# Optimization experiments

Measured on AMD Instinct MI355X. Metric: run time of the kernel, lower is better.

Reference implementation:

```python
import jax, jax.numpy as jnp
import numpy as np

B, NPG, IN_DIM, HID, H, DEG, NTYPE, NLAYERS = 4, 5000, 16, 128, 8, 32, 12, 4
N = B * NPG
DH = HID // H
E = N * DEG + N  # random edges + self loops


def setup_inputs() -> dict:
    key = jax.random.key(0)
    ks = jax.random.split(key, 10)
    e_rand = N * DEG
    # intra-graph random edges: sample within [0, NPG) then offset by graph id
    src = jax.random.randint(ks[0], (e_rand,), 0, NPG, dtype=jnp.int32)
    dst = jax.random.randint(ks[1], (e_rand,), 0, NPG, dtype=jnp.int32)
    gid = jnp.repeat(jnp.arange(B, dtype=jnp.int32), NPG * DEG) * NPG
    loops = jnp.arange(N, dtype=jnp.int32)
    edge_index = jnp.stack([jnp.concatenate([src + gid, loops]),
                            jnp.concatenate([dst + gid, loops])])
    edge_type = jnp.concatenate([
        jax.random.randint(ks[2], (e_rand,), 1, NTYPE, dtype=jnp.int32),
        jnp.zeros((N,), jnp.int32)])  # self-loop type = 0
    feat = jax.random.normal(ks[3], (N, IN_DIM), jnp.float32)
    s = 0.1
    return {
        "feat": feat,
        "edge_table": jax.random.normal(ks[4], (NTYPE, HID), jnp.float32) * s,
        "W_embed": jax.random.normal(ks[5], (IN_DIM, HID), jnp.float32) * s,
        "b_embed": jnp.zeros((HID,), jnp.float32),
        "W_conv": jax.random.normal(ks[6], (HID, HID), jnp.float32) * s,
        "a_src": jax.random.normal(ks[7], (H, DH), jnp.float32) * s,
        "a_dst": jax.random.normal(ks[8], (H, DH), jnp.float32) * s,
        "a_edge": jax.random.normal(ks[9], (H, DH), jnp.float32) * s,
        "edge_index": edge_index,
        "edge_type": edge_type,
    }


def _forward(feat, edge_table, W_embed, b_embed, W_conv, a_src, a_dst, a_edge,
             edge_index, edge_type):
    src, dst = edge_index[0], edge_index[1]
    # feature masking done in the torch forward
    feat = feat.at[:, 2:4].set(0.0).at[:, 10:].set(0.0)
    # 'sum'-flavor edge embedding: type lookup -> [E, H, DH]
    e_feat = edge_table[edge_type].reshape(-1, H, DH)
    ea = jnp.sum(e_feat * a_edge, axis=-1)  # [E, H]
    h = jax.nn.gelu(feat @ W_embed + b_embed)  # node embedder MLP
    layers = [feat, h]
    for _ in range(NLAYERS):  # shared_conv=True: same weights each layer
        z = (h @ W_conv).reshape(N, H, DH)
        s_logit = jnp.sum(z * a_src, axis=-1)  # [N, H]
        d_logit = jnp.sum(z * a_dst, axis=-1)
        logit = jax.nn.leaky_relu(s_logit[src] + d_logit[dst] + ea, 0.2)
        # numerically-stable edge softmax over incoming edges of each dst
        m = jax.ops.segment_max(logit, dst, num_segments=N)
        ex = jnp.exp(logit - jax.lax.stop_gradient(m)[dst])
        denom = jax.ops.segment_sum(ex, dst, num_segments=N)
        alpha = ex / (denom[dst] + 1e-9)  # [E, H]
        msg = alpha[..., None] * z[src]  # [E, H, DH]
        agg = jax.ops.segment_sum(msg, dst, num_segments=N).reshape(N, HID)
        h = h + jax.nn.gelu(agg)  # residual
        layers.append(h)
    feats_all = jnp.concatenate(layers, axis=1)  # layer_pooling='all' -> [N, 656]
    nf = feats_all.reshape(B, NPG, -1)
    g_emb = jnp.max(nf, axis=1, keepdims=True)  # graph_pooling='max'
    return jnp.concatenate([nf, jnp.broadcast_to(g_emb, nf.shape)], axis=2)


def reference(feat, edge_table, W_embed, b_embed, W_conv, a_src, a_dst, a_edge,
              edge_index, edge_type):
    return _forward(feat, edge_table, W_embed, b_embed, W_conv, a_src, a_dst,
                    a_edge, edge_index, edge_type)
```

## Files before the change

kernel.cpp:

```cpp
#include <hip/hip_runtime.h>
#include <math.h>

#define IN_DIM 16
#define HIDN 128
#define NH 8
#define DHD 16
#define NTYPE 12
#define NLAYERS 4
#define NPG 5000
#define NSEGP 250
#define RPS (NPG / NSEGP)
#define C1 656
#define C2 1312
#define C1Q (C1 / 4)
#define CAP 64
#define NPW 4
#define HREG (NPG / 2)
#define GEMM_SLOTS ((HREG + 63) / 64)
#define EDGE_SLOTS (HREG / NPW)

__device__ __forceinline__ float gelu_t(float x) {
    float x3 = x * x * x;
    float u = 0.7978845608028654f * (x + 0.044715f * x3);
    return 0.5f * x * (1.0f + tanhf(u));
}

__device__ __forceinline__ unsigned pack_bf16(float lo, float hi) {
    unsigned a = __float_as_uint(lo);
    unsigned b = __float_as_uint(hi);
    a = (a + 0x7fffu + ((a >> 16) & 1u)) >> 16;
    b = (b + 0x7fffu + ((b >> 16) & 1u)) & 0xffff0000u;
    return a | b;
}

__device__ __forceinline__ float lrelu(float x) { return (x >= 0.f) ? x : 0.2f * x; }

__global__ __launch_bounds__(256) void k_init(const float* __restrict__ etab,
                                              const float* __restrict__ aed,
                                              float* __restrict__ ea, int* __restrict__ cnt,
                                              int N) {
    int i = blockIdx.x * 256 + threadIdx.x;
    if (i < NTYPE * NH) {
        int t = i / NH, hh = i % NH;
        float s = 0.f;
        #pragma unroll
        for (int d = 0; d < DHD; d++) s += etab[t * HIDN + hh * DHD + d] * aed[hh * DHD + d];
        ea[i] = s;
    }
    if (i < N) cnt[i] = 0;
}

__global__ __launch_bounds__(256) void k_pre(const float* __restrict__ feat,
                                             const float* __restrict__ We,
                                             const float* __restrict__ be,
                                             const int* __restrict__ srcp,
                                             const int* __restrict__ dstp,
                                             const int* __restrict__ etp,
                                             int* __restrict__ cnt,
                                             unsigned* __restrict__ payload2,
                                             float* __restrict__ out, int N, int E) {
    int bid = blockIdx.x, tid = threadIdx.x;
    int wave = tid >> 6, lane = tid & 63;
    int n = bid * NPW + wave;
    if (n < N) {
        float v = 0.f;
        if (lane < IN_DIM) {
            v = feat[n * IN_DIM + lane];
            if ((lane >= 2 && lane < 4) || lane >= 10) v = 0.f;
            out[(size_t)n * C2 + lane] = v;
        }
        float a0 = be[lane], a1 = be[lane + 64];
        #pragma unroll
        for (int k = 0; k < IN_DIM; k++) {
            float fk = __shfl(v, k);
            a0 += fk * We[k * HIDN + lane];
            a1 += fk * We[k * HIDN + lane + 64];
        }
        size_t ob = (size_t)n * C2 + IN_DIM;
        out[ob + lane] = gelu_t(a0);
        out[ob + lane + 64] = gelu_t(a1);
    }
    for (int e = bid * 256 + tid; e < E; e += gridDim.x * 256) {
        int d = dstp[e];
        int slot = atomicAdd(&cnt[d], 1);
        if (slot < CAP)
            payload2[(size_t)d * CAP + slot] = (unsigned)srcp[e] | ((unsigned)etp[e] << 16);
    }
}

#define KC 64
__global__ __launch_bounds__(256) void k_gemm(const float* __restrict__ out,
                                              const float* __restrict__ W,
                                              const float* __restrict__ asf,
                                              const float* __restrict__ adf,
                                              unsigned* __restrict__ z16,
                                              float* __restrict__ slog,
                                              float* __restrict__ dlog, int prevbase, int N) {
    __shared__ float WcA[KC][64];
    __shared__ float WcB[KC][64];
    __shared__ float hc[64][KC + 4];
    int xcd = blockIdx.x & 7, slot = blockIdx.x >> 3;
    int g = xcd & 3, half = xcd >> 2;
    int base = g * NPG + half * HREG;
    int rend = base + HREG;
    int n0 = base + slot * 64;
    int t = threadIdx.x;
    int cg = t & 15, rg = t >> 4;
    int c0 = cg * 8;
    const float* hin = out + prevbase;
    float acc[4][8];
    #pragma unroll
    for (int i = 0; i < 4; i++)
        #pragma unroll
        for (int j = 0; j < 8; j++) acc[i][j] = 0.f;

    for (int k0 = 0; k0 < HIDN; k0 += KC) {
        for (int i = t; i < KC * 32; i += 256) {
            int kk = i >> 5, cc = (i & 31) << 2;
            float4 v = *(const float4*)&W[(k0 + kk) * HIDN + cc];
            int halfcol = (cc & ~4) >> 1;
            if (cc & 4) *(float4*)&WcB[kk][halfcol] = v;
            else *(float4*)&WcA[kk][halfcol] = v;
        }
        for (int i = t; i < 64 * (KC / 4); i += 256) {
            int rr = i / (KC / 4), kk = (i % (KC / 4)) * 4;
            int n = n0 + rr;
            float4 v = make_float4(0.f, 0.f, 0.f, 0.f);
            if (n < rend) v = *(const float4*)&hin[(size_t)n * C2 + k0 + kk];
            *(float4*)&hc[rr][kk] = v;
        }
        __syncthreads();
        for (int k = 0; k < KC; k++) {
            float4 w0 = *(float4*)&WcA[k][cg * 4];
            float4 w1 = *(float4*)&WcB[k][cg * 4];
            float hv[4];
            #pragma unroll
            for (int i = 0; i < 4; i++) hv[i] = hc[rg + 16 * i][k];
            #pragma unroll
            for (int i = 0; i < 4; i++) {
                acc[i][0] += hv[i] * w0.x;
                acc[i][1] += hv[i] * w0.y;
                acc[i][2] += hv[i] * w0.z;
                acc[i][3] += hv[i] * w0.w;
                acc[i][4] += hv[i] * w1.x;
                acc[i][5] += hv[i] * w1.y;
                acc[i][6] += hv[i] * w1.z;
                acc[i][7] += hv[i] * w1.w;
            }
        }
        __syncthreads();
    }
    float4 s0 = *(const float4*)&asf[c0];
    float4 s1 = *(const float4*)&asf[c0 + 4];
    float4 d0 = *(const float4*)&adf[c0];
    float4 d1 = *(const float4*)&adf[c0 + 4];
    #pragma unroll
    for (int i = 0; i < 4; i++) {
        int n = n0 + rg + 16 * i;
        float ps = acc[i][0] * s0.x + acc[i][1] * s0.y + acc[i][2] * s0.z + acc[i][3] * s0.w +
                   acc[i][4] * s1.x + acc[i][5] * s1.y + acc[i][6] * s1.z + acc[i][7] * s1.w;
        float pd = acc[i][0] * d0.x + acc[i][1] * d0.y + acc[i][2] * d0.z + acc[i][3] * d0.w +
                   acc[i][4] * d1.x + acc[i][5] * d1.y + acc[i][6] * d1.z + acc[i][7] * d1.w;
        ps += __shfl_xor(ps, 1);
        pd += __shfl_xor(pd, 1);
        unsigned u[8];
        #pragma unroll
        for (int j = 0; j < 8; j++) {
            float other = __shfl_xor(acc[i][j], 8);
            u[j] = pack_bf16(acc[i][j], other);
        }
        if (n < rend) {
            if (cg < 8) {
                *(uint4*)&z16[(size_t)n * 64 + c0] = make_uint4(u[0], u[1], u[2], u[3]);
                *(uint4*)&z16[(size_t)n * 64 + c0 + 4] = make_uint4(u[4], u[5], u[6], u[7]);
            }
            if ((cg & 1) == 0) {
                slog[n * NH + (cg >> 1)] = ps;
                dlog[n * NH + (cg >> 1)] = pd;
            }
        }
    }
}

__global__ __launch_bounds__(256) void k_edge(const int* __restrict__ cnt,
                                              const unsigned* __restrict__ payload2,
                                              const float* __restrict__ slog,
                                              const float* __restrict__ dlog,
                                              const float* __restrict__ ea,
                                              const unsigned* __restrict__ z16,
                                              float* __restrict__ out, int prevbase,
                                              int curbase, int N) {
    int wave = threadIdx.x >> 6, lane = threadIdx.x & 63;
    int xcd = blockIdx.x & 7, slot = blockIdx.x >> 3;
    int g = xcd & 3, half = xcd >> 2;
    int unit = g * (NPG / NPW) + half * EDGE_SLOTS + slot;
    int n = unit * NPW + wave;
    bool active = (n < N);
    __shared__ float lbuf[NPW][CAP * NH];
    __shared__ unsigned pbuf[NPW][CAP];
    __shared__ float dl[NPW][NH];
    __shared__ float red[NPW][NH];
    __shared__ float sea[NTYPE * NH];

    if (threadIdx.x < NTYPE * NH) sea[threadIdx.x] = ea[threadIdx.x];

    int cntE = 0;
    if (active) {
        cntE = cnt[n];
        if (cntE > CAP) cntE = CAP;
        if (lane < NH) dl[wave][lane] = dlog[n * NH + lane];
    }
    if (lane < cntE) pbuf[wave][lane] = payload2[(size_t)n * CAP + lane];
    __syncthreads();

    int o = lane & 1;
    int eoff = lane >> 1;
    float4 dl4 = *(float4*)&dl[wave][o * 4];
    float4 ssum4 = make_float4(0.f, 0.f, 0.f, 0.f);
    #pragma unroll
    for (int base = 0; base < CAP; base += 32) {
        int el = base + eoff;
        if (el < cntE) {
            unsigned pk = pbuf[wave][el];
            int src = pk & 0xffff;
            int et = pk >> 16;
            float4 s4 = *(const float4*)&slog[src * NH + o * 4];
            float4 e4 = *(float4*)&sea[et * NH + o * 4];
            float4 ex;
            ex.x = __expf(lrelu(s4.x + dl4.x + e4.x));
            ex.y = __expf(lrelu(s4.y + dl4.y + e4.y));
            ex.z = __expf(lrelu(s4.z + dl4.z + e4.z));
            ex.w = __expf(lrelu(s4.w + dl4.w + e4.w));
            *(float4*)&lbuf[wave][el * NH + o * 4] = ex;
            ssum4.x += ex.x;
            ssum4.y += ex.y;
            ssum4.z += ex.z;
            ssum4.w += ex.w;
        }
    }
    #pragma unroll
    for (int m = 2; m <= 32; m <<= 1) {
        ssum4.x += __shfl_xor(ssum4.x, m);
        ssum4.y += __shfl_xor(ssum4.y, m);
        ssum4.z += __shfl_xor(ssum4.z, m);
        ssum4.w += __shfl_xor(ssum4.w, m);
    }
    if (lane < 2) {
        float4 r4;
        r4.x = 1.0f / (ssum4.x + 1e-9f);
        r4.y = 1.0f / (ssum4.y + 1e-9f);
        r4.z = 1.0f / (ssum4.z + 1e-9f);
        r4.w = 1.0f / (ssum4.w + 1e-9f);
        *(float4*)&red[wave][o * 4] = r4;
    }
    __syncthreads();

    int h1 = lane >> 4, h2 = h1 + 4;
    float r1 = red[wave][h1], r2 = red[wave][h2];
    float a0 = 0.f, a1 = 0.f;
    int e = 0;
    for (; e + 7 < cntE; e += 8) {
        unsigned v[8];
        #pragma unroll
        for (int j = 0; j < 8; j++) {
            unsigned s = pbuf[wave][e + j] & 0xffff;
            v[j] = z16[(size_t)s * 64 + lane];
        }
        #pragma unroll
        for (int j = 0; j < 8; j++) {
            float l0 = lbuf[wave][(e + j) * NH + h1];
            float l1 = lbuf[wave][(e + j) * NH + h2];
            a0 += l0 * __uint_as_float(v[j] << 16);
            a1 += l1 * __uint_as_float(v[j] & 0xffff0000u);
        }
    }
    for (; e < cntE; e++) {
        unsigned s0 = pbuf[wave][e] & 0xffff;
        unsigned v0 = z16[(size_t)s0 * 64 + lane];
        a0 += lbuf[wave][e * NH + h1] * __uint_as_float(v0 << 16);
        a1 += lbuf[wave][e * NH + h2] * __uint_as_float(v0 & 0xffff0000u);
    }
    if (active) {
        a0 *= r1;
        a1 *= r2;
        size_t rowb = (size_t)n * C2;
        float o0 = out[rowb + prevbase + lane] + gelu_t(a0);
        float o1 = out[rowb + prevbase + lane + 64] + gelu_t(a1);
        out[rowb + curbase + lane] = o0;
        out[rowb + curbase + lane + 64] = o1;
    }
}

__global__ __launch_bounds__(256) void k_pool_partial(const float* __restrict__ out,
                                                      float* __restrict__ gpart) {
    int xcd = blockIdx.x & 7, slot = blockIdx.x >> 3;
    int b = xcd & 3, half = xcd >> 2;
    int seg = half * (NSEGP / 2) + slot;
    int n0 = b * NPG + seg * RPS;
    for (int c = threadIdx.x; c < C1; c += 256) {
        float m = -3.4e38f;
        #pragma unroll
        for (int i = 0; i < RPS; i++) m = fmaxf(m, out[(size_t)(n0 + i) * C2 + c]);
        gpart[(size_t)(b * NSEGP + seg) * C1 + c] = m;
    }
}

__global__ __launch_bounds__(256) void k_pool_final(const float* __restrict__ gpart,
                                                    float* __restrict__ gemb, int B) {
    int w = blockIdx.x * 4 + (threadIdx.x >> 6);
    int lane = threadIdx.x & 63;
    if (w >= B * C1) return;
    int b = w / C1, c = w % C1;
    float m = -3.4e38f;
    for (int s = lane; s < NSEGP; s += 64) m = fmaxf(m, gpart[(size_t)(b * NSEGP + s) * C1 + c]);
    #pragma unroll
    for (int k = 1; k < 64; k <<= 1) m = fmaxf(m, __shfl_xor(m, k));
    if (lane == 0) gemb[w] = m;
}

__global__ __launch_bounds__(256) void k_bcast(const float* __restrict__ gemb,
                                               float* __restrict__ out, int N) {
    int idx = blockIdx.x * 256 + threadIdx.x;
    if (idx < N * C1Q) {
        int n = idx / C1Q, c4 = idx % C1Q;
        int b = n / NPG;
        float4 g = *(const float4*)&gemb[b * C1 + c4 * 4];
        *(float4*)&out[(size_t)n * C2 + C1 + c4 * 4] = g;
    }
}

extern "C" void kernel_launch(void* const* d_in, const int* in_sizes, int n_in, void* d_out,
                              int out_size, void* d_ws, size_t ws_size, hipStream_t stream) {
    const float* feat = (const float*)d_in[0];
    const float* etab = (const float*)d_in[1];
    const float* We = (const float*)d_in[2];
    const float* be = (const float*)d_in[3];
    const float* Wc = (const float*)d_in[4];
    const float* a_src = (const float*)d_in[5];
    const float* a_dst = (const float*)d_in[6];
    const float* a_edge = (const float*)d_in[7];
    const int* eidx = (const int*)d_in[8];
    const int* etype = (const int*)d_in[9];
    float* out = (float*)d_out;

    const int N = in_sizes[0] / IN_DIM;
    const int E = in_sizes[9];
    const int B = N / NPG;

    const int* srcp = eidx;
    const int* dstp = eidx + E;

    char* w = (char*)d_ws;
    size_t off = 0;
    auto carve = [&](size_t bytes) {
        char* p = w + off;
        off = (off + bytes + 255) & ~(size_t)255;
        return p;
    };
    unsigned* z16 = (unsigned*)carve((size_t)N * 64 * 4);
    float* slog = (float*)carve((size_t)N * NH * 4);
    float* dlog = (float*)carve((size_t)N * NH * 4);
    float* ea = (float*)carve(NTYPE * NH * 4);
    int* cnt = (int*)carve((size_t)N * 4);
    unsigned* payload2 = (unsigned*)carve((size_t)N * CAP * 4);
    float* gpart = (float*)carve((size_t)B * NSEGP * C1 * 4);
    float* gemb = (float*)carve((size_t)B * C1 * 4);
    (void)ws_size;

    k_init<<<(N + 255) / 256, 256, 0, stream>>>(etab, a_edge, ea, cnt, N);
    k_pre<<<(N + NPW - 1) / NPW, 256, 0, stream>>>(feat, We, be, srcp, dstp, etype, cnt,
                                                   payload2, out, N, E);

    for (int l = 0; l < NLAYERS; l++) {
        int prevbase = IN_DIM + HIDN * l;
        int curbase = IN_DIM + HIDN * (l + 1);
        k_gemm<<<8 * GEMM_SLOTS, 256, 0, stream>>>(out, Wc, a_src, a_dst, z16, slog, dlog,
                                                   prevbase, N);
        k_edge<<<8 * EDGE_SLOTS, 256, 0, stream>>>(cnt, payload2, slog, dlog, ea, z16, out,
                                                   prevbase, curbase, N);
    }

    k_pool_partial<<<8 * (NSEGP / 2), 256, 0, stream>>>(out, gpart);
    k_pool_final<<<(B * C1 + 3) / 4, 256, 0, stream>>>(gpart, gemb, B);
    k_bcast<<<((size_t)N * C1Q + 255) / 256, 256, 0, stream>>>(gemb, out, N);
}
```

Before: 251.5 us.

## Fuse graph max-pooling into producer kernels via atomicMax keys; shrink GEMM row tile

The max-pool over each graph's nodes is folded into k_pre and k_edge. Each block reduces its four rows in shared memory and does an atomicMax on an order-preserving unsigned key per graph column. This removes the two pooling kernels and the second full read of the first 656 output columns. Separately, the GEMM row tile drops from 64 to 32 rows, doubling the number of blocks for better occupancy at the cost of less W reuse per block. The atomics add contention on a small key array, and k_pre's graph index assumes a block never straddles two graphs.

```diff
diff --git a/kernel.cpp b/kernel.cpp
--- a/kernel.cpp
+++ b/kernel.cpp
@@ -8,15 +8,14 @@
 #define NTYPE 12
 #define NLAYERS 4
 #define NPG 5000
-#define NSEGP 250
-#define RPS (NPG / NSEGP)
 #define C1 656
 #define C2 1312
 #define C1Q (C1 / 4)
 #define CAP 64
 #define NPW 4
 #define HREG (NPG / 2)
-#define GEMM_SLOTS ((HREG + 63) / 64)
+#define GROWS 32
+#define GEMM_SLOTS ((HREG + GROWS - 1) / GROWS)
 #define EDGE_SLOTS (HREG / NPW)
 
 __device__ __forceinline__ float gelu_t(float x) {
@@ -35,10 +34,18 @@
 
 __device__ __forceinline__ float lrelu(float x) { return (x >= 0.f) ? x : 0.2f * x; }
 
+__device__ __forceinline__ unsigned fkey(float x) {
+    unsigned b = __float_as_uint(x);
+    return (b & 0x80000000u) ? ~b : (b | 0x80000000u);
+}
+__device__ __forceinline__ float funkey(unsigned k) {
+    return __uint_as_float((k & 0x80000000u) ? (k ^ 0x80000000u) : ~k);
+}
+
 __global__ __launch_bounds__(256) void k_init(const float* __restrict__ etab,
                                               const float* __restrict__ aed,
                                               float* __restrict__ ea, int* __restrict__ cnt,
-                                              int N) {
+                                              unsigned* __restrict__ gkeys, int N) {
     int i = blockIdx.x * 256 + threadIdx.x;
     if (i < NTYPE * NH) {
         int t = i / NH, hh = i % NH;
@@ -48,6 +55,7 @@
         ea[i] = s;
     }
     if (i < N) cnt[i] = 0;
+    if (i < 4 * C1) gkeys[i] = 0u;
 }
 
 __global__ __launch_bounds__(256) void k_pre(const float* __restrict__ feat,
@@ -58,12 +66,14 @@
                                              const int* __restrict__ etp,
                                              int* __restrict__ cnt,
                                              unsigned* __restrict__ payload2,
+                                             unsigned* __restrict__ gkeys,
                                              float* __restrict__ out, int N, int E) {
     int bid = blockIdx.x, tid = threadIdx.x;
     int wave = tid >> 6, lane = tid & 63;
+    __shared__ float pm[NPW][IN_DIM + HIDN];
     int n = bid * NPW + wave;
+    float v = 0.f;
     if (n < N) {
-        float v = 0.f;
         if (lane < IN_DIM) {
             v = feat[n * IN_DIM + lane];
             if ((lane >= 2 && lane < 4) || lane >= 10) v = 0.f;
@@ -76,9 +86,23 @@
             a0 += fk * We[k * HIDN + lane];
             a1 += fk * We[k * HIDN + lane + 64];
         }
+        float g0 = gelu_t(a0), g1 = gelu_t(a1);
         size_t ob = (size_t)n * C2 + IN_DIM;
-        out[ob + lane] = gelu_t(a0);
-        out[ob + lane + 64] = gelu_t(a1);
+        out[ob + lane] = g0;
+        out[ob + lane + 64] = g1;
+        if (lane < IN_DIM) pm[wave][lane] = v;
+        pm[wave][IN_DIM + lane] = g0;
+        pm[wave][IN_DIM + lane + 64] = g1;
+    } else {
+        if (lane < IN_DIM) pm[wave][lane] = -3.4e38f;
+        pm[wave][IN_DIM + lane] = -3.4e38f;
+        pm[wave][IN_DIM + lane + 64] = -3.4e38f;
+    }
+    __syncthreads();
+    if (tid < IN_DIM + HIDN) {
+        float m = fmaxf(fmaxf(pm[0][tid], pm[1][tid]), fmaxf(pm[2][tid], pm[3][tid]));
+        int g = (bid * NPW) / NPG;
+        atomicMax(&gkeys[g * C1 + tid], fkey(m));
     }
     for (int e = bid * 256 + tid; e < E; e += gridDim.x * 256) {
         int d = dstp[e];
@@ -98,19 +122,19 @@
                                               float* __restrict__ dlog, int prevbase, int N) {
     __shared__ float WcA[KC][64];
     __shared__ float WcB[KC][64];
-    __shared__ float hc[64][KC + 4];
+    __shared__ float hc[GROWS][KC + 4];
     int xcd = blockIdx.x & 7, slot = blockIdx.x >> 3;
     int g = xcd & 3, half = xcd >> 2;
     int base = g * NPG + half * HREG;
     int rend = base + HREG;
-    int n0 = base + slot * 64;
+    int n0 = base + slot * GROWS;
     int t = threadIdx.x;
     int cg = t & 15, rg = t >> 4;
     int c0 = cg * 8;
     const float* hin = out + prevbase;
-    float acc[4][8];
+    float acc[2][8];
     #pragma unroll
-    for (int i = 0; i < 4; i++)
+    for (int i = 0; i < 2; i++)
         #pragma unroll
         for (int j = 0; j < 8; j++) acc[i][j] = 0.f;
 
@@ -122,8 +146,8 @@
             if (cc & 4) *(float4*)&WcB[kk][halfcol] = v;
             else *(float4*)&WcA[kk][halfcol] = v;
         }
-        for (int i = t; i < 64 * (KC / 4); i += 256) {
-            int rr = i / (KC / 4), kk = (i % (KC / 4)) * 4;
+        for (int i = t; i < GROWS * (KC / 4); i += 256) {
+            int rr = i >> 4, kk = (i & 15) * 4;
             int n = n0 + rr;
             float4 v = make_float4(0.f, 0.f, 0.f, 0.f);
             if (n < rend) v = *(const float4*)&hin[(size_t)n * C2 + k0 + kk];
@@ -133,11 +157,11 @@
         for (int k = 0; k < KC; k++) {
             float4 w0 = *(float4*)&WcA[k][cg * 4];
             float4 w1 = *(float4*)&WcB[k][cg * 4];
-            float hv[4];
+            float hv[2];
             #pragma unroll
-            for (int i = 0; i < 4; i++) hv[i] = hc[rg + 16 * i][k];
+            for (int i = 0; i < 2; i++) hv[i] = hc[rg + 16 * i][k];
             #pragma unroll
-            for (int i = 0; i < 4; i++) {
+            for (int i = 0; i < 2; i++) {
                 acc[i][0] += hv[i] * w0.x;
                 acc[i][1] += hv[i] * w0.y;
                 acc[i][2] += hv[i] * w0.z;
@@ -155,7 +179,7 @@
     float4 d0 = *(const float4*)&adf[c0];
     float4 d1 = *(const float4*)&adf[c0 + 4];
     #pragma unroll
-    for (int i = 0; i < 4; i++) {
+    for (int i = 0; i < 2; i++) {
         int n = n0 + rg + 16 * i;
         float ps = acc[i][0] * s0.x + acc[i][1] * s0.y + acc[i][2] * s0.z + acc[i][3] * s0.w +
                    acc[i][4] * s1.x + acc[i][5] * s1.y + acc[i][6] * s1.z + acc[i][7] * s1.w;
@@ -188,6 +212,7 @@
                                               const float* __restrict__ dlog,
                                               const float* __restrict__ ea,
                                               const unsigned* __restrict__ z16,
+                                              unsigned* __restrict__ gkeys,
                                               float* __restrict__ out, int prevbase,
                                               int curbase, int N) {
     int wave = threadIdx.x >> 6, lane = threadIdx.x & 63;
@@ -201,6 +226,7 @@
     __shared__ float dl[NPW][NH];
     __shared__ float red[NPW][NH];
     __shared__ float sea[NTYPE * NH];
+    __shared__ float pm[NPW][HIDN];
 
     if (threadIdx.x < NTYPE * NH) sea[threadIdx.x] = ea[threadIdx.x];
 
@@ -288,43 +314,32 @@
         float o1 = out[rowb + prevbase + lane + 64] + gelu_t(a1);
         out[rowb + curbase + lane] = o0;
         out[rowb + curbase + lane + 64] = o1;
-    }
-}
-
-__global__ __launch_bounds__(256) void k_pool_partial(const float* __restrict__ out,
-                                                      float* __restrict__ gpart) {
-    int xcd = blockIdx.x & 7, slot = blockIdx.x >> 3;
-    int b = xcd & 3, half = xcd >> 2;
-    int seg = half * (NSEGP / 2) + slot;
-    int n0 = b * NPG + seg * RPS;
-    for (int c = threadIdx.x; c < C1; c += 256) {
-        float m = -3.4e38f;
-        #pragma unroll
-        for (int i = 0; i < RPS; i++) m = fmaxf(m, out[(size_t)(n0 + i) * C2 + c]);
-        gpart[(size_t)(b * NSEGP + seg) * C1 + c] = m;
-    }
-}
-
-__global__ __launch_bounds__(256) void k_pool_final(const float* __restrict__ gpart,
-                                                    float* __restrict__ gemb, int B) {
-    int w = blockIdx.x * 4 + (threadIdx.x >> 6);
-    int lane = threadIdx.x & 63;
-    if (w >= B * C1) return;
-    int b = w / C1, c = w % C1;
-    float m = -3.4e38f;
-    for (int s = lane; s < NSEGP; s += 64) m = fmaxf(m, gpart[(size_t)(b * NSEGP + s) * C1 + c]);
-    #pragma unroll
-    for (int k = 1; k < 64; k <<= 1) m = fmaxf(m, __shfl_xor(m, k));
-    if (lane == 0) gemb[w] = m;
-}
-
-__global__ __launch_bounds__(256) void k_bcast(const float* __restrict__ gemb,
+        pm[wave][lane] = o0;
+        pm[wave][lane + 64] = o1;
+    } else {
+        pm[wave][lane] = -3.4e38f;
+        pm[wave][lane + 64] = -3.4e38f;
+    }
+    __syncthreads();
+    if (threadIdx.x < HIDN) {
+        float m = fmaxf(fmaxf(pm[0][threadIdx.x], pm[1][threadIdx.x]),
+                        fmaxf(pm[2][threadIdx.x], pm[3][threadIdx.x]));
+        atomicMax(&gkeys[g * C1 + curbase + threadIdx.x], fkey(m));
+    }
+}
+
+__global__ __launch_bounds__(256) void k_bcast(const unsigned* __restrict__ gkeys,
                                                float* __restrict__ out, int N) {
     int idx = blockIdx.x * 256 + threadIdx.x;
     if (idx < N * C1Q) {
         int n = idx / C1Q, c4 = idx % C1Q;
         int b = n / NPG;
-        float4 g = *(const float4*)&gemb[b * C1 + c4 * 4];
+        uint4 k4 = *(const uint4*)&gkeys[b * C1 + c4 * 4];
+        float4 g;
+        g.x = funkey(k4.x);
+        g.y = funkey(k4.y);
+        g.z = funkey(k4.z);
+        g.w = funkey(k4.w);
         *(float4*)&out[(size_t)n * C2 + C1 + c4 * 4] = g;
     }
 }
@@ -345,7 +360,6 @@
 
     const int N = in_sizes[0] / IN_DIM;
     const int E = in_sizes[9];
-    const int B = N / NPG;
 
     const int* srcp = eidx;
     const int* dstp = eidx + E;
@@ -363,24 +377,21 @@
     float* ea = (float*)carve(NTYPE * NH * 4);
     int* cnt = (int*)carve((size_t)N * 4);
     unsigned* payload2 = (unsigned*)carve((size_t)N * CAP * 4);
-    float* gpart = (float*)carve((size_t)B * NSEGP * C1 * 4);
-    float* gemb = (float*)carve((size_t)B * C1 * 4);
+    unsigned* gkeys = (unsigned*)carve((size_t)4 * C1 * 4);
     (void)ws_size;
 
-    k_init<<<(N + 255) / 256, 256, 0, stream>>>(etab, a_edge, ea, cnt, N);
+    k_init<<<(N + 255) / 256, 256, 0, stream>>>(etab, a_edge, ea, cnt, gkeys, N);
     k_pre<<<(N + NPW - 1) / NPW, 256, 0, stream>>>(feat, We, be, srcp, dstp, etype, cnt,
-                                                   payload2, out, N, E);
+                                                   payload2, gkeys, out, N, E);
 
     for (int l = 0; l < NLAYERS; l++) {
         int prevbase = IN_DIM + HIDN * l;
         int curbase = IN_DIM + HIDN * (l + 1);
         k_gemm<<<8 * GEMM_SLOTS, 256, 0, stream>>>(out, Wc, a_src, a_dst, z16, slog, dlog,
                                                    prevbase, N);
-        k_edge<<<8 * EDGE_SLOTS, 256, 0, stream>>>(cnt, payload2, slog, dlog, ea, z16, out,
-                                                   prevbase, curbase, N);
-    }
-
-    k_pool_partial<<<8 * (NSEGP / 2), 256, 0, stream>>>(out, gpart);
-    k_pool_final<<<(B * C1 + 3) / 4, 256, 0, stream>>>(gpart, gemb, B);
-    k_bcast<<<((size_t)N * C1Q + 255) / 256, 256, 0, stream>>>(gemb, out, N);
-}
+        k_edge<<<8 * EDGE_SLOTS, 256, 0, stream>>>(cnt, payload2, slog, dlog, ea, z16, gkeys,
+                                                   out, prevbase, curbase, N);
+    }
+
+    k_bcast<<<((size_t)N * C1Q + 255) / 256, 256, 0, stream>>>(gkeys, out, N);
+}
```

After: 294.2 us. 1.17x slower.
